# Optimization experiments

Hardware: AMD Instinct MI355X
Metric: run time of the kernel (lower is better)

The kernel has to match this reference:

```python
import jax, jax.numpy as jnp
import numpy as np

B, W, C, E, H, V = 128, 128, 32, 20, 64, 256


def setup_inputs() -> dict:
    key = jax.random.key(0)
    ks = jax.random.split(key, 12)
    # sentence lengths (in words) and word lengths (in chars); pads appended
    sent_lens = jax.random.randint(ks[0], (B,), 1, W + 1)
    word_valid = jnp.arange(W)[None, :] < sent_lens[:, None]            # [B,W]
    raw_lens = jax.random.randint(ks[1], (B, W), 1, C + 1)
    lengths = jnp.where(word_valid, raw_lens, 0)                        # [B,W]
    vals = jax.random.randint(ks[2], (B, W, C), 1, V)
    chars = jnp.where(jnp.arange(C)[None, None, :] < lengths[..., None], vals, 0).astype(jnp.int32)
    emb_table = (jax.random.normal(ks[3], (V, E), jnp.float32) * 0.1).at[0].set(0.0)  # padding_idx=0 row is zero
    def xavier(k, shape):
        fan_in, fan_out = shape[1], shape[0]
        lim = np.sqrt(6.0 / (fan_in + fan_out))
        return jax.random.uniform(k, shape, jnp.float32, -lim, lim)
    return dict(
        chars=chars,
        emb_table=emb_table,
        w_ih_f=xavier(ks[4], (4 * H, E)), w_hh_f=xavier(ks[5], (4 * H, H)),
        b_ih_f=jnp.zeros((4 * H,), jnp.float32), b_hh_f=jnp.zeros((4 * H,), jnp.float32),
        w_ih_b=xavier(ks[6], (4 * H, E)), w_hh_b=xavier(ks[7], (4 * H, H)),
        b_ih_b=jnp.zeros((4 * H,), jnp.float32), b_hh_b=jnp.zeros((4 * H,), jnp.float32),
    )


def _char_bilstm_words(chars, emb_table, w_ih_f, w_hh_f, b_ih_f, b_hh_f,
                       w_ih_b, w_hh_b, b_ih_b, b_hh_b):
    Bn, Wn, Cn = chars.shape
    Hn = w_hh_f.shape[1]
    x = emb_table[chars]                              # [B,W,C,E]
    lengths = jnp.sum(chars != 0, axis=-1)            # [B,W]; padding char embeds to 0
    N = Bn * Wn
    xf = x.reshape(N, Cn, -1)                         # flatten all words: [N,C,E]
    lens = lengths.reshape(N)
    bias_f = b_ih_f + b_hh_f

    def step(carry, x_t):
        h, c = carry
        g = x_t @ w_ih_f.T + h @ w_hh_f.T + bias_f    # [N,4H], torch gate order i,f,g,o
        i, f, gg, o = jnp.split(g, 4, axis=-1)
        c = jax.nn.sigmoid(f) * c + jax.nn.sigmoid(i) * jnp.tanh(gg)
        h = jax.nn.sigmoid(o) * jnp.tanh(c)
        return (h, c), h

    h0 = jnp.zeros((N, Hn), x.dtype)
    _, hs = jax.lax.scan(step, (h0, h0), xf.transpose(1, 0, 2))   # [C,N,H]
    idx = jnp.maximum(lens - 1, 0)
    h_fwd = hs[idx, jnp.arange(N)]                                # fwd hidden at last valid char
    # backward direction output at t=len-1: one LSTM step on the last char from zero state
    x_last = jnp.take_along_axis(xf, idx[:, None, None], axis=1)[:, 0, :]   # [N,E]
    gb = x_last @ w_ih_b.T + (b_ih_b + b_hh_b)
    ib, fb, ggb, ob = jnp.split(gb, 4, axis=-1)
    cb = jax.nn.sigmoid(ib) * jnp.tanh(ggb)                       # f gate * 0 initial cell drops out
    h_bwd = jax.nn.sigmoid(ob) * jnp.tanh(cb)
    out = jnp.concatenate([h_fwd, h_bwd], axis=-1)                # [N,2H]
    out = out * (lens > 0)[:, None].astype(out.dtype)             # pad words -> zeros
    return out.reshape(Bn, Wn, 2 * Hn)


def reference(chars, emb_table, w_ih_f, w_hh_f, b_ih_f, b_hh_f,
              w_ih_b, w_hh_b, b_ih_b, b_hh_b):
    return _char_bilstm_words(chars, emb_table, w_ih_f, w_hh_f, b_ih_f, b_hh_f,
                              w_ih_b, w_hh_b, b_ih_b, b_hh_b)
```

## Files before the change

### kernel.cpp

```cpp
#include <hip/hip_runtime.h>
#include <hip/hip_bf16.h>
#include <stdint.h>

#define LOG2E 1.4426950408889634f

typedef float f32x2 __attribute__((ext_vector_type(2)));

__device__ __forceinline__ float fast_sig(float x) {
    float e = __builtin_amdgcn_exp2f(-LOG2E * x);
    return __builtin_amdgcn_rcpf(1.0f + e);
}
__device__ __forceinline__ float fast_tanh(float x) {
    float e = __builtin_amdgcn_exp2f(2.0f * LOG2E * x);
    return 1.0f - 2.0f * __builtin_amdgcn_rcpf(e + 1.0f);
}
__device__ __forceinline__ float rl_f(float v, int k) {
    return __int_as_float(__builtin_amdgcn_readlane(__float_as_int(v), k));
}

__global__ void prep1(const float* __restrict__ emb,
                      const float* __restrict__ w_ih_f, const float* __restrict__ b_ih_f,
                      const float* __restrict__ b_hh_f,
                      const float* __restrict__ w_ih_b, const float* __restrict__ b_ih_b,
                      const float* __restrict__ b_hh_b,
                      const float* __restrict__ w_hh_f, const int* __restrict__ chars,
                      float* __restrict__ xproj, float* __restrict__ hbwd,
                      float* __restrict__ wt, int* __restrict__ cnt,
                      int* __restrict__ lens) {
    const int blk = blockIdx.x, tid = threadIdx.x;
    if (blk < 64) {
        int d = blk * 256 + tid;
        int tk = d >> 8, tj = (d >> 2) & 63, tg = d & 3;
        wt[d] = w_hh_f[(((tg << 6) | tj) << 6) | tk];

        int v = blk * 4 + (tid >> 6);
        int j = tid & 63;
        float e[20];
#pragma unroll
        for (int t = 0; t < 20; ++t) e[t] = emb[v * 20 + t];
        float sf[4], sb[4];
#pragma unroll
        for (int g = 0; g < 4; ++g) {
            int row = g * 64 + j;
            float a = b_ih_f[row] + b_hh_f[row];
            float b = b_ih_b[row] + b_hh_b[row];
#pragma unroll
            for (int t = 0; t < 20; ++t) {
                a += e[t] * w_ih_f[row * 20 + t];
                b += e[t] * w_ih_b[row * 20 + t];
            }
            sf[g] = a; sb[g] = b;
        }
        ((float4*)xproj)[v * 64 + j] = make_float4(sf[0], sf[1], sf[2], sf[3]);
        float cb = fast_sig(sb[0]) * fast_tanh(sb[2]);
        hbwd[v * 64 + j] = fast_sig(sb[3]) * fast_tanh(cb);
    } else {
        int word = (blk - 64) * 8 + (tid >> 5);
        int c = tid & 31;
        int v = chars[word * 32 + c];
        unsigned long long m = __ballot(v != 0);
        int hi = (tid >> 5) & 1;
        int len = __popcll(m & (hi ? 0xFFFFFFFF00000000ULL : 0x00000000FFFFFFFFULL));
        if (c == 0) {
            lens[word] = len;
            if (len > 0) atomicAdd(&cnt[len], 1);
        }
    }
}

__global__ void prep2(const int* __restrict__ lens, const int* __restrict__ cnt,
                      int* __restrict__ cursor0, int* __restrict__ sorted,
                      int* __restrict__ nvp, float4* __restrict__ out4) {
    int word = blockIdx.x * 8 + (threadIdx.x >> 5);
    int c = threadIdx.x & 31;
    int len = lens[word];
    if (len == 0) {
        out4[word * 32 + c] = make_float4(0.f, 0.f, 0.f, 0.f);
    } else if (c == 0) {
        int pre = 0;
        for (int l = len + 1; l <= 32; ++l) pre += cnt[l];
        int pos = pre + atomicAdd(&cursor0[len], 1);
        sorted[pos] = word;
    }
    if (word == 0 && c == 1) {
        int t = 0;
        for (int l = 1; l <= 32; ++l) t += cnt[l];
        *nvp = t;
    }
}

__launch_bounds__(256, 2)
__global__ void bilstm_main(const int* __restrict__ chars, const float4* __restrict__ wtv,
                            const float4* __restrict__ xproj, const float* __restrict__ hbwd,
                            const int* __restrict__ sorted, const int* __restrict__ nvp,
                            float* __restrict__ out) {
    __shared__ float4 ldsw[3584];
    const int nv = *nvp;
    const int chunks = (nv + 3) >> 2;
    const int B = (chunks + 3) >> 2;
    if ((int)blockIdx.x >= B) return;
    const int tid = threadIdx.x;
    for (int i = tid; i < 3584; i += 256) ldsw[i] = wtv[512 + i];
    __syncthreads();

    const int wave = tid >> 6, lane = tid & 63;
    const int cidx = (int)blockIdx.x + wave * B;
    const int base = cidx * 4;
    const int nw = min(4, nv - base);
    if (nw <= 0) return;

    float4 wreg[8];
#pragma unroll
    for (int i = 0; i < 8; ++i) wreg[i] = wtv[i * 64 + lane];

    int idv = 0;
    if (lane < 4 && base + lane < nv) idv = sorted[base + lane];

    int wid[4], ch[4], len[4];
#pragma unroll
    for (int g = 0; g < 4; ++g) {
        wid[g] = __builtin_amdgcn_readlane(idv, g);
        int c = 0;
        if (lane < 32) c = chars[wid[g] * 32 + lane];
        ch[g] = c;
        unsigned long long m = __ballot(c != 0);
        len[g] = (g < nw) ? __popcll(m) : 0;
    }
    int maxlen = 0;
#pragma unroll
    for (int g = 0; g < 4; ++g) maxlen = max(maxlen, len[g]);

    float h[4], cc[4];
#pragma unroll
    for (int g = 0; g < 4; ++g) { h[g] = 0.0f; cc[g] = 0.0f; }

    for (int t = 0; t < maxlen; ++t) {
        f32x2 axy[4], azw[4];
#pragma unroll
        for (int g = 0; g < 4; ++g) {
            int ct = __builtin_amdgcn_readlane(ch[g], t);
            float4 xp = xproj[ct * 64 + lane];
            axy[g][0] = xp.x; axy[g][1] = xp.y;
            azw[g][0] = xp.z; azw[g][1] = xp.w;
        }
#pragma unroll
        for (int k = 0; k < 8; ++k) {
            float4 w4 = wreg[k];
            f32x2 wxy; wxy[0] = w4.x; wxy[1] = w4.y;
            f32x2 wzw; wzw[0] = w4.z; wzw[1] = w4.w;
#pragma unroll
            for (int g = 0; g < 4; ++g) {
                float hk = rl_f(h[g], k);
                f32x2 h2; h2[0] = hk; h2[1] = hk;
                axy[g] = __builtin_elementwise_fma(h2, wxy, axy[g]);
                azw[g] = __builtin_elementwise_fma(h2, wzw, azw[g]);
            }
        }
#pragma unroll 8
        for (int k = 8; k < 64; ++k) {
            float4 w4 = ldsw[((k - 8) << 6) + lane];
            f32x2 wxy; wxy[0] = w4.x; wxy[1] = w4.y;
            f32x2 wzw; wzw[0] = w4.z; wzw[1] = w4.w;
#pragma unroll
            for (int g = 0; g < 4; ++g) {
                float hk = rl_f(h[g], k);
                f32x2 h2; h2[0] = hk; h2[1] = hk;
                axy[g] = __builtin_elementwise_fma(h2, wxy, axy[g]);
                azw[g] = __builtin_elementwise_fma(h2, wzw, azw[g]);
            }
        }
#pragma unroll
        for (int g = 0; g < 4; ++g) {
            float gi = fast_sig(axy[g][0]);
            float gf = fast_sig(axy[g][1]);
            float gg = fast_tanh(azw[g][0]);
            float go = fast_sig(azw[g][1]);
            float cn = gf * cc[g] + gi * gg;
            float hn = go * fast_tanh(cn);
            bool act = (t < len[g]);
            cc[g] = act ? cn : cc[g];
            h[g] = act ? hn : h[g];
        }
    }

#pragma unroll
    for (int g = 0; g < 4; ++g) {
        if (g < nw) {
            int cl = __builtin_amdgcn_readlane(ch[g], len[g] - 1);
            float hb = hbwd[cl * 64 + lane];
            out[wid[g] * 128 + lane] = h[g];
            out[wid[g] * 128 + 64 + lane] = hb;
        }
    }
}

extern "C" void kernel_launch(void* const* d_in, const int* in_sizes, int n_in,
                              void* d_out, int out_size, void* d_ws, size_t ws_size,
                              hipStream_t stream) {
    const int* chars    = (const int*)d_in[0];
    const float* emb    = (const float*)d_in[1];
    const float* w_ih_f = (const float*)d_in[2];
    const float* w_hh_f = (const float*)d_in[3];
    const float* b_ih_f = (const float*)d_in[4];
    const float* b_hh_f = (const float*)d_in[5];
    const float* w_ih_b = (const float*)d_in[6];
    const float* b_ih_b = (const float*)d_in[8];
    const float* b_hh_b = (const float*)d_in[9];
    float* out = (float*)d_out;

    float* wsf   = (float*)d_ws;
    float* xproj = wsf;
    float* hbwd  = wsf + 65536;
    float* wt    = wsf + 65536 + 16384;
    int* iws     = (int*)(wt + 16384);
    int* sorted  = iws;
    int* lens    = iws + 16384;
    int* cnt     = iws + 32768;
    int* cursor0 = iws + 33792;
    int* nv      = iws + 33856;

    (void)hipMemsetAsync(cnt, 0, 33 * sizeof(int), stream);
    (void)hipMemsetAsync(cursor0, 0, 65 * sizeof(int), stream);
    prep1<<<2112, 256, 0, stream>>>(emb, w_ih_f, b_ih_f, b_hh_f,
                                    w_ih_b, b_ih_b, b_hh_b, w_hh_f, chars,
                                    xproj, hbwd, wt, cnt, lens);
    prep2<<<2048, 256, 0, stream>>>(lens, cnt, cursor0, sorted, nv, (float4*)out);
    bilstm_main<<<1024, 256, 0, stream>>>(chars, (const float4*)wt,
                                          (const float4*)xproj,
                                          hbwd, sorted, nv, out);
}
```

Measured before the change: 223.8 us.

## Balance LSTM work across waves by total character count instead of fixed chunks

Replaces the fixed four-word chunk per wave with a work partition in which each of 2048 waves takes a contiguous range of length-sorted words covering an equal share of the total character steps, computed from the length histogram. Each wave loops over groups of four words in its range. The aim is to remove tail imbalance, since waves holding long words previously dominated while others sat idle, and to halve the grid so the weight-load prologue is amortised over more words. Every wave now rescans the histogram, and the range boundaries can split groups so that they hold words of mixed length.

```diff
diff --git a/kernel.cpp b/kernel.cpp
--- a/kernel.cpp
+++ b/kernel.cpp
@@ -70,7 +70,7 @@
 
 __global__ void prep2(const int* __restrict__ lens, const int* __restrict__ cnt,
                       int* __restrict__ cursor0, int* __restrict__ sorted,
-                      int* __restrict__ nvp, float4* __restrict__ out4) {
+                      float4* __restrict__ out4) {
     int word = blockIdx.x * 8 + (threadIdx.x >> 5);
     int c = threadIdx.x & 31;
     int len = lens[word];
@@ -82,114 +82,124 @@
         int pos = pre + atomicAdd(&cursor0[len], 1);
         sorted[pos] = word;
     }
-    if (word == 0 && c == 1) {
-        int t = 0;
-        for (int l = 1; l <= 32; ++l) t += cnt[l];
-        *nvp = t;
-    }
 }
 
 __launch_bounds__(256, 2)
 __global__ void bilstm_main(const int* __restrict__ chars, const float4* __restrict__ wtv,
                             const float4* __restrict__ xproj, const float* __restrict__ hbwd,
-                            const int* __restrict__ sorted, const int* __restrict__ nvp,
+                            const int* __restrict__ sorted, const int* __restrict__ cnt,
                             float* __restrict__ out) {
     __shared__ float4 ldsw[3584];
-    const int nv = *nvp;
-    const int chunks = (nv + 3) >> 2;
-    const int B = (chunks + 3) >> 2;
-    if ((int)blockIdx.x >= B) return;
     const int tid = threadIdx.x;
     for (int i = tid; i < 3584; i += 256) ldsw[i] = wtv[512 + i];
     __syncthreads();
 
     const int wave = tid >> 6, lane = tid & 63;
-    const int cidx = (int)blockIdx.x + wave * B;
-    const int base = cidx * 4;
-    const int nw = min(4, nv - base);
-    if (nw <= 0) return;
 
     float4 wreg[8];
 #pragma unroll
     for (int i = 0; i < 8; ++i) wreg[i] = wtv[i * 64 + lane];
 
-    int idv = 0;
-    if (lane < 4 && base + lane < nv) idv = sorted[base + lane];
-
-    int wid[4], ch[4], len[4];
-#pragma unroll
-    for (int g = 0; g < 4; ++g) {
-        wid[g] = __builtin_amdgcn_readlane(idv, g);
-        int c = 0;
-        if (lane < 32) c = chars[wid[g] * 32 + lane];
-        ch[g] = c;
-        unsigned long long m = __ballot(c != 0);
-        len[g] = (g < nw) ? __popcll(m) : 0;
-    }
-    int maxlen = 0;
-#pragma unroll
-    for (int g = 0; g < 4; ++g) maxlen = max(maxlen, len[g]);
-
-    float h[4], cc[4];
-#pragma unroll
-    for (int g = 0; g < 4; ++g) { h[g] = 0.0f; cc[g] = 0.0f; }
-
-    for (int t = 0; t < maxlen; ++t) {
-        f32x2 axy[4], azw[4];
+    const int myw = (int)blockIdx.x * 4 + wave;
+    unsigned S = 0;
+    for (int l = 1; l <= 32; ++l) S += (unsigned)cnt[l] * (unsigned)l;
+    unsigned T0 = ((unsigned)myw * S) >> 11;
+    unsigned T1 = ((unsigned)(myw + 1) * S) >> 11;
+    int p0 = -1, p1 = -1;
+    {
+        unsigned CS = 0, CW = 0;
+        for (int l = 32; l >= 1; --l) {
+            unsigned c = (unsigned)cnt[l];
+            unsigned seg = c * (unsigned)l;
+            if (p0 < 0 && T0 < CS + seg) p0 = (int)(CW + (T0 - CS) / (unsigned)l);
+            if (p1 < 0 && T1 < CS + seg) p1 = (int)(CW + (T1 - CS) / (unsigned)l);
+            CS += seg; CW += c;
+        }
+        if (p0 < 0) p0 = (int)CW;
+        if (p1 < 0) p1 = (int)CW;
+    }
+
+    for (int base = p0; base < p1; base += 4) {
+        const int nw = min(4, p1 - base);
+
+        int idv = 0;
+        if (lane < 4 && base + lane < p1) idv = sorted[base + lane];
+
+        int wid[4], ch[4], len[4];
 #pragma unroll
         for (int g = 0; g < 4; ++g) {
-            int ct = __builtin_amdgcn_readlane(ch[g], t);
-            float4 xp = xproj[ct * 64 + lane];
-            axy[g][0] = xp.x; axy[g][1] = xp.y;
-            azw[g][0] = xp.z; azw[g][1] = xp.w;
-        }
-#pragma unroll
-        for (int k = 0; k < 8; ++k) {
-            float4 w4 = wreg[k];
-            f32x2 wxy; wxy[0] = w4.x; wxy[1] = w4.y;
-            f32x2 wzw; wzw[0] = w4.z; wzw[1] = w4.w;
+            wid[g] = __builtin_amdgcn_readlane(idv, g);
+            int c = 0;
+            if (lane < 32) c = chars[wid[g] * 32 + lane];
+            ch[g] = c;
+            unsigned long long m = __ballot(c != 0);
+            len[g] = (g < nw) ? __popcll(m) : 0;
+        }
+        int maxlen = 0;
+#pragma unroll
+        for (int g = 0; g < 4; ++g) maxlen = max(maxlen, len[g]);
+
+        float h[4], cc[4];
+#pragma unroll
+        for (int g = 0; g < 4; ++g) { h[g] = 0.0f; cc[g] = 0.0f; }
+
+        for (int t = 0; t < maxlen; ++t) {
+            f32x2 axy[4], azw[4];
 #pragma unroll
             for (int g = 0; g < 4; ++g) {
-                float hk = rl_f(h[g], k);
-                f32x2 h2; h2[0] = hk; h2[1] = hk;
-                axy[g] = __builtin_elementwise_fma(h2, wxy, axy[g]);
-                azw[g] = __builtin_elementwise_fma(h2, wzw, azw[g]);
-            }
-        }
+                int ct = __builtin_amdgcn_readlane(ch[g], t);
+                float4 xp = xproj[ct * 64 + lane];
+                axy[g][0] = xp.x; axy[g][1] = xp.y;
+                azw[g][0] = xp.z; azw[g][1] = xp.w;
+            }
+#pragma unroll
+            for (int k = 0; k < 8; ++k) {
+                float4 w4 = wreg[k];
+                f32x2 wxy; wxy[0] = w4.x; wxy[1] = w4.y;
+                f32x2 wzw; wzw[0] = w4.z; wzw[1] = w4.w;
+#pragma unroll
+                for (int g = 0; g < 4; ++g) {
+                    float hk = rl_f(h[g], k);
+                    f32x2 h2; h2[0] = hk; h2[1] = hk;
+                    axy[g] = __builtin_elementwise_fma(h2, wxy, axy[g]);
+                    azw[g] = __builtin_elementwise_fma(h2, wzw, azw[g]);
+                }
+            }
 #pragma unroll 8
-        for (int k = 8; k < 64; ++k) {
-            float4 w4 = ldsw[((k - 8) << 6) + lane];
-            f32x2 wxy; wxy[0] = w4.x; wxy[1] = w4.y;
-            f32x2 wzw; wzw[0] = w4.z; wzw[1] = w4.w;
+            for (int k = 8; k < 64; ++k) {
+                float4 w4 = ldsw[((k - 8) << 6) + lane];
+                f32x2 wxy; wxy[0] = w4.x; wxy[1] = w4.y;
+                f32x2 wzw; wzw[0] = w4.z; wzw[1] = w4.w;
+#pragma unroll
+                for (int g = 0; g < 4; ++g) {
+                    float hk = rl_f(h[g], k);
+                    f32x2 h2; h2[0] = hk; h2[1] = hk;
+                    axy[g] = __builtin_elementwise_fma(h2, wxy, axy[g]);
+                    azw[g] = __builtin_elementwise_fma(h2, wzw, azw[g]);
+                }
+            }
 #pragma unroll
             for (int g = 0; g < 4; ++g) {
-                float hk = rl_f(h[g], k);
-                f32x2 h2; h2[0] = hk; h2[1] = hk;
-                axy[g] = __builtin_elementwise_fma(h2, wxy, axy[g]);
-                azw[g] = __builtin_elementwise_fma(h2, wzw, azw[g]);
-            }
-        }
+                float gi = fast_sig(axy[g][0]);
+                float gf = fast_sig(axy[g][1]);
+                float gg = fast_tanh(azw[g][0]);
+                float go = fast_sig(azw[g][1]);
+                float cn = gf * cc[g] + gi * gg;
+                float hn = go * fast_tanh(cn);
+                bool act = (t < len[g]);
+                cc[g] = act ? cn : cc[g];
+                h[g] = act ? hn : h[g];
+            }
+        }
+
 #pragma unroll
         for (int g = 0; g < 4; ++g) {
-            float gi = fast_sig(axy[g][0]);
-            float gf = fast_sig(axy[g][1]);
-            float gg = fast_tanh(azw[g][0]);
-            float go = fast_sig(azw[g][1]);
-            float cn = gf * cc[g] + gi * gg;
-            float hn = go * fast_tanh(cn);
-            bool act = (t < len[g]);
-            cc[g] = act ? cn : cc[g];
-            h[g] = act ? hn : h[g];
-        }
-    }
-
-#pragma unroll
-    for (int g = 0; g < 4; ++g) {
-        if (g < nw) {
-            int cl = __builtin_amdgcn_readlane(ch[g], len[g] - 1);
-            float hb = hbwd[cl * 64 + lane];
-            out[wid[g] * 128 + lane] = h[g];
-            out[wid[g] * 128 + 64 + lane] = hb;
+            if (g < nw) {
+                int cl = __builtin_amdgcn_readlane(ch[g], len[g] - 1);
+                float hb = hbwd[cl * 64 + lane];
+                out[wid[g] * 128 + lane] = h[g];
+                out[wid[g] * 128 + 64 + lane] = hb;
+            }
         }
     }
 }
@@ -217,15 +227,14 @@
     int* lens    = iws + 16384;
     int* cnt     = iws + 32768;
     int* cursor0 = iws + 33792;
-    int* nv      = iws + 33856;
 
     (void)hipMemsetAsync(cnt, 0, 33 * sizeof(int), stream);
-    (void)hipMemsetAsync(cursor0, 0, 65 * sizeof(int), stream);
+    (void)hipMemsetAsync(cursor0, 0, 33 * sizeof(int), stream);
     prep1<<<2112, 256, 0, stream>>>(emb, w_ih_f, b_ih_f, b_hh_f,
                                     w_ih_b, b_ih_b, b_hh_b, w_hh_f, chars,
                                     xproj, hbwd, wt, cnt, lens);
-    prep2<<<2048, 256, 0, stream>>>(lens, cnt, cursor0, sorted, nv, (float4*)out);
-    bilstm_main<<<1024, 256, 0, stream>>>(chars, (const float4*)wt,
-                                          (const float4*)xproj,
-                                          hbwd, sorted, nv, out);
-}
+    prep2<<<2048, 256, 0, stream>>>(lens, cnt, cursor0, sorted, (float4*)out);
+    bilstm_main<<<512, 256, 0, stream>>>(chars, (const float4*)wt,
+                                         (const float4*)xproj,
+                                         hbwd, sorted, cnt, out);
+}
```

Result: slower. 238.5 us (+6.5%).
